# Optimization experiments

Measured on AMD Instinct MI355X. Metric: run time of the kernel, lower is better.

The kernel has to match this reference:

```python
import jax, jax.numpy as jnp
import numpy as np

INPUT_DIM, HIDDEN, CB_DIM, CB_SIZE = 768, 512, 256, 512
COMMIT_W = 1.0


def setup_inputs() -> dict:
    key = jax.random.key(0)
    ks = jax.random.split(key, 10)
    def lin(k, fan_in, fan_out):
        lim = 1.0 / np.sqrt(fan_in)
        return jax.random.uniform(k, (fan_in, fan_out), jnp.float32, -lim, lim)
    return {
        "x": jax.random.normal(ks[0], (32, 2048, INPUT_DIM), jnp.float32),
        "W1": lin(ks[1], INPUT_DIM, HIDDEN),
        "b1": jnp.zeros((HIDDEN,), jnp.float32),
        "W2": lin(ks[2], HIDDEN, CB_DIM),
        "b2": jnp.zeros((CB_DIM,), jnp.float32),
        "codebook": jax.random.normal(ks[3], (CB_SIZE, CB_DIM), jnp.float32),
        "W3": lin(ks[4], CB_DIM, HIDDEN),
        "b3": jnp.zeros((HIDDEN,), jnp.float32),
        "W4": lin(ks[5], HIDDEN, INPUT_DIM),
        "b4": jnp.zeros((INPUT_DIM,), jnp.float32),
    }


def reference(x, W1, b1, W2, b2, codebook, W3, b3, W4, b4):
    # encoder MLP: [b, n, 768] -> [b, n, 256]
    h = jax.nn.relu(jnp.einsum('bnd,dh->bnh', x, W1) + b1)
    z = jnp.einsum('bnh,hc->bnc', h, W2) + b2

    # VQ: squared-L2 distance to codebook, argmin, gather
    # d(z, c) = ||z||^2 - 2 z.c + ||c||^2  (||z||^2 constant over argmin, omitted)
    dots = jnp.einsum('bnc,kc->bnk', z, codebook)          # [b, n, K]
    c_sq = jnp.sum(codebook * codebook, axis=-1)            # [K]
    indices = jnp.argmin(c_sq - 2.0 * dots, axis=-1)        # [b, n] int
    q = codebook[indices]                                   # [b, n, 256] gather

    # straight-through estimator + commitment loss
    quantized = z + jax.lax.stop_gradient(q - z)
    commit_loss = COMMIT_W * jnp.mean((z - jax.lax.stop_gradient(q)) ** 2)

    # decoder MLP: [b, n, 256] -> [b, n, 768]
    h2 = jax.nn.relu(jnp.einsum('bnc,ch->bnh', quantized, W3) + b3)
    recon = jnp.einsum('bnh,hd->bnd', h2, W4) + b4
    return recon, indices.astype(jnp.int32), commit_loss
```

## Files before the change

### kernel.cpp

```cpp
#include <hip/hip_runtime.h>

typedef unsigned short u16;
typedef unsigned int   u32;
typedef __attribute__((ext_vector_type(8))) short short8;
typedef __attribute__((ext_vector_type(4))) float f32x4;

#define NTOK 65536
#define IND  768
#define HID  512
#define CBD  256
#define CBS  512

#define OUT_IDX_OFF   ((size_t)NTOK * IND)
#define OUT_LOSS_OFF  (OUT_IDX_OFF + NTOK)

#define OFF_H      ((size_t)0)
#define OFF_Z      ((size_t)134217728)
#define OFF_W1H    ((size_t)201326592)
#define OFF_W1L    ((size_t)202113024)
#define OFF_W2H    ((size_t)202899456)
#define OFF_W2L    ((size_t)203161600)
#define OFF_CBH    ((size_t)203423744)
#define OFF_CBL    ((size_t)203685888)
#define OFF_CSQ    ((size_t)203948032)
#define OFF_PART   ((size_t)0)
#define OFF_TABLE  ((size_t)8388608)
#define OFF_ZSQ    ((size_t)9961472)
#define OFF_IDX    ((size_t)10223616)
#define OFF_FLAGS  ((size_t)10485760)
#define OFF_CNT    ((size_t)10747904)

__device__ __forceinline__ u16 f2bf(float f) {
    u32 u = __float_as_uint(f);
    return (u16)((u + 0x7fffu + ((u >> 16) & 1u)) >> 16);
}
__device__ __forceinline__ float bf2f(u16 h) {
    return __uint_as_float(((u32)h) << 16);
}

__global__ __launch_bounds__(256) void cbsplit(
    const float* __restrict__ cb, u16* __restrict__ hi, u16* __restrict__ lo,
    float* __restrict__ csq)
{
    int c = blockIdx.x, t = threadIdx.x;
    float v = cb[(size_t)c * CBD + t];
    u16 h = f2bf(v); u16 l = f2bf(v - bf2f(h));
    hi[(size_t)c * CBD + t] = h; lo[(size_t)c * CBD + t] = l;
    __shared__ float red[256];
    red[t] = v * v; __syncthreads();
    for (int s = 128; s; s >>= 1) { if (t < s) red[t] += red[t + s]; __syncthreads(); }
    if (!t) csq[c] = red[0];
}

__global__ __launch_bounds__(256) void wsplit(
    const float* __restrict__ W, u16* __restrict__ hi, u16* __restrict__ lo,
    int K, int N)
{
    int n = blockIdx.x;
    for (int k = threadIdx.x; k < K; k += 256) {
        float v = W[(size_t)k * N + n];
        u16 h = f2bf(v); u16 l = f2bf(v - bf2f(h));
        hi[(size_t)n * K + k] = h; lo[(size_t)n * K + k] = l;
    }
}

template<int AMODE, int EPI>
__global__ __launch_bounds__(256, 2) void gemm3(
    const float* __restrict__ Af, const u32* __restrict__ Apk,
    const u16* __restrict__ Bhi, const u16* __restrict__ Blo,
    const float* __restrict__ bias,
    u32* __restrict__ Opk, float* __restrict__ Opart,
    int M, int N, int K)
{
    __shared__ u16 lds[4 * 128 * 40];
    u16* sAh = lds;
    u16* sAl = lds + 5120;
    u16* sBh = lds + 10240;
    u16* sBl = lds + 15360;
    const int tid  = threadIdx.x;
    const int m0 = blockIdx.y * 128, n0 = blockIdx.x * 128;
    const int w = tid >> 6, lane = tid & 63, quad = lane >> 4, l15 = lane & 15;
    const int wm = (w & 1) * 64, wn = (w >> 1) * 64;

    f32x4 acc[4][4] = {};

    for (int k0 = 0; k0 < K; k0 += 32) {
        __syncthreads();
        if (AMODE == 0) {
            #pragma unroll
            for (int s = 0; s < 4; ++s) {
                int slot = tid + s * 256;
                int m = slot >> 3, kg = (slot & 7) << 2;
                float4 v = *(const float4*)(Af + (size_t)(m0 + m) * K + k0 + kg);
                u16 h0 = f2bf(v.x), h1 = f2bf(v.y), h2 = f2bf(v.z), h3 = f2bf(v.w);
                ushort4 hv = {h0, h1, h2, h3};
                ushort4 lv = {f2bf(v.x - bf2f(h0)), f2bf(v.y - bf2f(h1)),
                              f2bf(v.z - bf2f(h2)), f2bf(v.w - bf2f(h3))};
                *(ushort4*)&sAh[m * 40 + kg] = hv;
                *(ushort4*)&sAl[m * 40 + kg] = lv;
            }
        } else {
            #pragma unroll
            for (int s = 0; s < 4; ++s) {
                int slot = tid + s * 256;
                int m = slot >> 3, ke = (slot & 7) << 2;
                uint4 u = *(const uint4*)(Apk + (size_t)(m0 + m) * K + k0 + ke);
                ushort4 hv = {(u16)(u.x & 0xffff), (u16)(u.y & 0xffff),
                              (u16)(u.z & 0xffff), (u16)(u.w & 0xffff)};
                ushort4 lv = {(u16)(u.x >> 16), (u16)(u.y >> 16),
                              (u16)(u.z >> 16), (u16)(u.w >> 16)};
                *(ushort4*)&sAh[m * 40 + ke] = hv;
                *(ushort4*)&sAl[m * 40 + ke] = lv;
            }
        }
        #pragma unroll
        for (int s = 0; s < 4; ++s) {
            int slot = tid + s * 256;
            int n = (slot & 511) >> 2, ku = slot & 3;
            const u16* src = (slot < 512) ? Bhi : Blo;
            u16* dst = (slot < 512) ? sBh : sBl;
            uint4 u = *(const uint4*)(src + (size_t)(n0 + n) * K + k0 + ku * 8);
            *(uint4*)&dst[n * 40 + ku * 8] = u;
        }
        __syncthreads();

        short8 ah[4], al[4], bh[4], bl[4];
        const int ko = quad * 8;
        #pragma unroll
        for (int i = 0; i < 4; ++i) {
            int ar = wm + i * 16 + l15;
            int br = wn + i * 16 + l15;
            ah[i] = *(const short8*)&sAh[ar * 40 + ko];
            al[i] = *(const short8*)&sAl[ar * 40 + ko];
            bh[i] = *(const short8*)&sBh[br * 40 + ko];
            bl[i] = *(const short8*)&sBl[br * 40 + ko];
        }
        #pragma unroll
        for (int i = 0; i < 4; ++i)
            #pragma unroll
            for (int j = 0; j < 4; ++j) {
                acc[i][j] = __builtin_amdgcn_mfma_f32_16x16x32_bf16(ah[i], bh[j], acc[i][j], 0, 0, 0);
                acc[i][j] = __builtin_amdgcn_mfma_f32_16x16x32_bf16(ah[i], bl[j], acc[i][j], 0, 0, 0);
                acc[i][j] = __builtin_amdgcn_mfma_f32_16x16x32_bf16(al[i], bh[j], acc[i][j], 0, 0, 0);
            }
    }

    if (EPI <= 1) {
        float bn[4];
        #pragma unroll
        for (int j = 0; j < 4; ++j) bn[j] = bias[n0 + wn + j * 16 + l15];
        #pragma unroll
        for (int i = 0; i < 4; ++i)
            #pragma unroll
            for (int r = 0; r < 4; ++r) {
                int row = m0 + wm + i * 16 + quad * 4 + r;
                #pragma unroll
                for (int j = 0; j < 4; ++j) {
                    float v = acc[i][j][r] + bn[j];
                    if (EPI == 0) v = fmaxf(v, 0.f);
                    u16 h = f2bf(v); u16 l = f2bf(v - bf2f(h));
                    Opk[(size_t)row * N + n0 + wn + j * 16 + l15] = (u32)h | ((u32)l << 16);
                }
            }
    } else {
        float cs[4]; int cidx[4];
        #pragma unroll
        for (int j = 0; j < 4; ++j) {
            cidx[j] = n0 + wn + j * 16 + l15;
            cs[j] = bias[cidx[j]];
        }
        const int nparts = gridDim.x * 2;
        const int pslot  = blockIdx.x * 2 + (w >> 1);
        #pragma unroll
        for (int i = 0; i < 4; ++i)
            #pragma unroll
            for (int r = 0; r < 4; ++r) {
                int row = m0 + wm + i * 16 + quad * 4 + r;
                float d1 = 3.4e38f, d2 = 3.4e38f; int i1 = 0x7fffffff;
                #pragma unroll
                for (int j = 0; j < 4; ++j) {
                    float v = fmaf(-2.0f, acc[i][j][r], cs[j]);
                    if (v < d1) { d2 = d1; d1 = v; i1 = cidx[j]; }
                    else d2 = fminf(d2, v);
                }
                #pragma unroll
                for (int mm = 1; mm < 16; mm <<= 1) {
                    float od1 = __shfl_xor(d1, mm, 64);
                    float od2 = __shfl_xor(d2, mm, 64);
                    int   oi1 = __shfl_xor(i1, mm, 64);
                    if (od1 < d1 || (od1 == d1 && oi1 < i1)) { d2 = fminf(d1, od2); d1 = od1; i1 = oi1; }
                    else d2 = fminf(d2, od1);
                }
                if (l15 == 0) {
                    float4 o = {d1, d2, __int_as_float(i1), 0.f};
                    *(float4*)&Opart[((size_t)row * nparts + pslot) * 4] = o;
                }
            }
    }
}

__global__ __launch_bounds__(256) void zsq_pk(
    const u32* __restrict__ Zpk, float* __restrict__ zsq)
{
    int tok = blockIdx.x * 4 + (threadIdx.x >> 6);
    int lane = threadIdx.x & 63;
    uint4 u = *(const uint4*)(Zpk + (size_t)tok * CBD + lane * 4);
    float z0 = bf2f((u16)(u.x & 0xffff)) + bf2f((u16)(u.x >> 16));
    float z1 = bf2f((u16)(u.y & 0xffff)) + bf2f((u16)(u.y >> 16));
    float z2 = bf2f((u16)(u.z & 0xffff)) + bf2f((u16)(u.z >> 16));
    float z3 = bf2f((u16)(u.w & 0xffff)) + bf2f((u16)(u.w >> 16));
    float s = z0 * z0 + z1 * z1 + z2 * z2 + z3 * z3;
    #pragma unroll
    for (int off = 32; off; off >>= 1) s += __shfl_down(s, off, 64);
    if (!lane) zsq[tok] = s;
}

__global__ __launch_bounds__(256) void vq_reduce(
    const float* __restrict__ part, const float* __restrict__ zsq,
    float* __restrict__ out_idx, int* __restrict__ idx_i,
    int* __restrict__ cnt, float* __restrict__ accum, int* __restrict__ flags)
{
    int tok = blockIdx.x * 256 + threadIdx.x;
    float d1 = 3.4e38f, d2 = 3.4e38f; int i1 = 0x7fffffff;
    #pragma unroll
    for (int nb = 0; nb < 8; ++nb) {
        float4 p = *(const float4*)&part[((size_t)tok * 8 + nb) * 4];
        float pd1 = p.x, pd2 = p.y; int pi1 = __float_as_int(p.z);
        if (pd1 < d1 || (pd1 == d1 && pi1 < i1)) { d2 = fminf(d1, pd2); d1 = pd1; i1 = pi1; }
        else d2 = fminf(d2, pd1);
    }
    out_idx[tok] = (float)i1;
    idx_i[tok] = i1;
    if (d2 - d1 < 0.05f) {
        int p = atomicAdd(cnt, 1);
        if (p >= 0 && p < NTOK) flags[p] = tok;
    }
    float c = zsq[tok] + d1;
    __shared__ float red[256];
    red[threadIdx.x] = c; __syncthreads();
    for (int s = 128; s; s >>= 1) { if (threadIdx.x < s) red[threadIdx.x] += red[threadIdx.x + s]; __syncthreads(); }
    if (!threadIdx.x) atomicAdd(accum, red[0]);
}

__global__ __launch_bounds__(256) void fixup(
    const int* __restrict__ cnt, const int* __restrict__ flags,
    const float* __restrict__ x, const float* __restrict__ W1, const float* __restrict__ b1,
    const float* __restrict__ W2, const float* __restrict__ b2,
    const float* __restrict__ cb, const float* __restrict__ csq,
    int* __restrict__ idx_i, float* __restrict__ out_idx)
{
    __shared__ float xs[IND], hs[HID], zs[CBD], ds[CBS];
    int n = cnt[0]; if (n > NTOK) n = NTOK; if (n < 0) n = 0;
    int t = threadIdx.x;
    for (int it = blockIdx.x; it < n; it += gridDim.x) {
        int tok = flags[it];
        if (t < 192) *(float4*)&xs[t * 4] = *(const float4*)(x + (size_t)tok * IND + t * 4);
        __syncthreads();
        #pragma unroll
        for (int s2 = 0; s2 < 2; ++s2) {
            int j = t + s2 * 256; float a = b1[j];
            for (int k = 0; k < IND; ++k) a = fmaf(xs[k], W1[(size_t)k * HID + j], a);
            hs[j] = fmaxf(a, 0.f);
        }
        __syncthreads();
        {
            float a = b2[t];
            for (int k = 0; k < HID; ++k) a = fmaf(hs[k], W2[(size_t)k * CBD + t], a);
            zs[t] = a;
        }
        __syncthreads();
        {
            int wv = t >> 6, l = t & 63;
            float4 zv = *(const float4*)&zs[l * 4];
            for (int cc = 0; cc < 128; ++cc) {
                int c = wv * 128 + cc;
                float4 cv = *(const float4*)(cb + (size_t)c * CBD + l * 4);
                float p = zv.x * cv.x + zv.y * cv.y + zv.z * cv.z + zv.w * cv.w;
                #pragma unroll
                for (int mm = 32; mm; mm >>= 1) p += __shfl_xor(p, mm, 64);
                if (!l) ds[c] = csq[c] - 2.f * p;
            }
        }
        __syncthreads();
        if (t < 64) {
            float bd = ds[t]; int bi = t;
            for (int c = t + 64; c < CBS; c += 64) {
                float d = ds[c];
                if (d < bd || (d == bd && c < bi)) { bd = d; bi = c; }
            }
            #pragma unroll
            for (int mm = 1; mm < 64; mm <<= 1) {
                float od = __shfl_xor(bd, mm, 64); int oi = __shfl_xor(bi, mm, 64);
                if (od < bd || (od == bd && oi < bi)) { bd = od; bi = oi; }
            }
            if (!t) { idx_i[tok] = bi; out_idx[tok] = (float)bi; }
        }
        __syncthreads();
    }
}

__global__ __launch_bounds__(256) void table_pre(
    const float* __restrict__ cb, const float* __restrict__ W3,
    const float* __restrict__ b3, const float* __restrict__ W4,
    const float* __restrict__ b4, float* __restrict__ table)
{
    __shared__ float crow[CBD];
    __shared__ float h2[HID];
    const int c = blockIdx.x;
    const int t = threadIdx.x;
    crow[t] = cb[(size_t)c * CBD + t];
    __syncthreads();
    #pragma unroll
    for (int s = 0; s < 2; ++s) {
        int j = t + s * 256;
        float acc = b3[j];
        for (int k = 0; k < CBD; ++k) acc = fmaf(crow[k], W3[(size_t)k * HID + j], acc);
        h2[j] = fmaxf(acc, 0.f);
    }
    __syncthreads();
    #pragma unroll
    for (int s = 0; s < 3; ++s) {
        int j = t + s * 256;
        float acc = b4[j];
        for (int k = 0; k < HID; ++k) acc = fmaf(h2[k], W4[(size_t)k * IND + j], acc);
        table[(size_t)c * IND + j] = acc;
    }
}

__global__ __launch_bounds__(256) void gather_kernel(
    const int* __restrict__ idx, const float* __restrict__ table,
    float* __restrict__ out)
{
    unsigned i = blockIdx.x * 256u + threadIdx.x;
    unsigned tok = i / 192u;
    unsigned c = i - tok * 192u;
    int id = idx[tok];
    ((float4*)out)[i] = ((const float4*)table)[(size_t)id * 192 + c];
}

__global__ void finalize_kernel(const float* __restrict__ accum,
                                float* __restrict__ out_loss)
{
    out_loss[0] = accum[0] * (1.0f / 16777216.0f);
}

extern "C" void kernel_launch(void* const* d_in, const int* in_sizes, int n_in,
                              void* d_out, int out_size, void* d_ws, size_t ws_size,
                              hipStream_t stream) {
    const float* x  = (const float*)d_in[0];
    const float* W1 = (const float*)d_in[1];
    const float* b1 = (const float*)d_in[2];
    const float* W2 = (const float*)d_in[3];
    const float* b2 = (const float*)d_in[4];
    const float* cb = (const float*)d_in[5];
    const float* W3 = (const float*)d_in[6];
    const float* b3 = (const float*)d_in[7];
    const float* W4 = (const float*)d_in[8];
    const float* b4 = (const float*)d_in[9];

    char* ws = (char*)d_ws;
    u32*  Hpk   = (u32*)(ws + OFF_H);
    u32*  Zpk   = (u32*)(ws + OFF_Z);
    u16*  W1h   = (u16*)(ws + OFF_W1H);
    u16*  W1l   = (u16*)(ws + OFF_W1L);
    u16*  W2h   = (u16*)(ws + OFF_W2H);
    u16*  W2l   = (u16*)(ws + OFF_W2L);
    u16*  CBh   = (u16*)(ws + OFF_CBH);
    u16*  CBl   = (u16*)(ws + OFF_CBL);
    float* csq  = (float*)(ws + OFF_CSQ);
    float* part = (float*)(ws + OFF_PART);
    float* table = (float*)(ws + OFF_TABLE);
    float* zsq  = (float*)(ws + OFF_ZSQ);
    int*   idx_i = (int*)(ws + OFF_IDX);
    int*   flags = (int*)(ws + OFF_FLAGS);
    int*   cnt   = (int*)(ws + OFF_CNT);
    float* accum = (float*)(ws + OFF_CNT + 4);

    float* out      = (float*)d_out;
    float* out_idx  = out + OUT_IDX_OFF;
    float* out_loss = out + OUT_LOSS_OFF;

    cbsplit<<<CBS, 256, 0, stream>>>(cb, CBh, CBl, csq);
    wsplit<<<HID, 256, 0, stream>>>(W1, W1h, W1l, IND, HID);
    wsplit<<<CBD, 256, 0, stream>>>(W2, W2h, W2l, HID, CBD);

    gemm3<0, 0><<<dim3(HID / 128, NTOK / 128), 256, 0, stream>>>(
        x, (const u32*)nullptr, W1h, W1l, b1, Hpk, (float*)nullptr, NTOK, HID, IND);
    gemm3<1, 1><<<dim3(CBD / 128, NTOK / 128), 256, 0, stream>>>(
        (const float*)nullptr, Hpk, W2h, W2l, b2, Zpk, (float*)nullptr, NTOK, CBD, HID);

    hipMemsetAsync(cnt, 0, 8, stream);

    zsq_pk<<<NTOK / 4, 256, 0, stream>>>(Zpk, zsq);

    gemm3<1, 2><<<dim3(CBS / 128, NTOK / 128), 256, 0, stream>>>(
        (const float*)nullptr, Zpk, CBh, CBl, csq, (u32*)nullptr, part, NTOK, CBS, CBD);

    table_pre<<<CBS, 256, 0, stream>>>(cb, W3, b3, W4, b4, table);

    vq_reduce<<<NTOK / 256, 256, 0, stream>>>(part, zsq, out_idx, idx_i, cnt, accum, flags);

    fixup<<<192, 256, 0, stream>>>(cnt, flags, x, W1, b1, W2, b2, cb, csq, idx_i, out_idx);

    gather_kernel<<<(NTOK * (IND / 4)) / 256, 256, 0, stream>>>(idx_i, table, out);

    finalize_kernel<<<1, 1, 0, stream>>>(accum, out_loss);
}
```

Baseline: 1.019 ms.

## Batch eight flagged tokens per block in FP32 VQ fixup kernel

The fixup kernel recomputes the encoder and codebook argmin in exact FP32 for tokens whose top-two distances are close. It now handles eight tokens per block iteration, so each W1, W2 and codebook element loaded from global memory is reused across eight tokens instead of one. The argmin now runs as a per-wave running minimum instead of going through a shared distance array. The launch grid grows from 192 to 1024 blocks. Shared memory per block and register pressure rise, and when few tokens are flagged the padded batches do redundant work.

After: 984.9 us. 3.4% less time.

```diff
diff --git a/kernel.cpp b/kernel.cpp
--- a/kernel.cpp
+++ b/kernel.cpp
@@ -249,51 +249,115 @@
     const float* __restrict__ cb, const float* __restrict__ csq,
     int* __restrict__ idx_i, float* __restrict__ out_idx)
 {
-    __shared__ float xs[IND], hs[HID], zs[CBD], ds[CBS];
+    __shared__ float xs[8][IND];
+    __shared__ float hs[8][HID];
+    __shared__ float zs[8][CBD];
+    __shared__ float bd_s[4][8];
+    __shared__ int   bi_s[4][8];
+    __shared__ int   tok_s[8];
+
     int n = cnt[0]; if (n > NTOK) n = NTOK; if (n < 0) n = 0;
-    int t = threadIdx.x;
-    for (int it = blockIdx.x; it < n; it += gridDim.x) {
-        int tok = flags[it];
-        if (t < 192) *(float4*)&xs[t * 4] = *(const float4*)(x + (size_t)tok * IND + t * 4);
-        __syncthreads();
-        #pragma unroll
-        for (int s2 = 0; s2 < 2; ++s2) {
-            int j = t + s2 * 256; float a = b1[j];
-            for (int k = 0; k < IND; ++k) a = fmaf(xs[k], W1[(size_t)k * HID + j], a);
-            hs[j] = fmaxf(a, 0.f);
-        }
-        __syncthreads();
+    const int t = threadIdx.x;
+    const int nb = (n + 7) >> 3;
+
+    for (int ib = blockIdx.x; ib < nb; ib += gridDim.x) {
+        const int base = ib * 8;
+        if (t < 8) {
+            int fi = base + t; if (fi > n - 1) fi = n - 1;
+            tok_s[t] = flags[fi];
+        }
+        __syncthreads();
+
+        #pragma unroll
+        for (int s = 0; s < 6; ++s) {
+            int slot = t + s * 256;
+            int tt = slot / 192, c4 = slot - tt * 192;
+            *(float4*)&xs[tt][c4 * 4] =
+                *(const float4*)(x + (size_t)tok_s[tt] * IND + c4 * 4);
+        }
+        __syncthreads();
+
         {
-            float a = b2[t];
-            for (int k = 0; k < HID; ++k) a = fmaf(hs[k], W2[(size_t)k * CBD + t], a);
-            zs[t] = a;
-        }
-        __syncthreads();
+            float a0[8], a1[8];
+            float bb0 = b1[t], bb1 = b1[t + 256];
+            #pragma unroll
+            for (int tt = 0; tt < 8; ++tt) { a0[tt] = bb0; a1[tt] = bb1; }
+            #pragma unroll 4
+            for (int k = 0; k < IND; ++k) {
+                float w0 = W1[(size_t)k * HID + t];
+                float w1 = W1[(size_t)k * HID + t + 256];
+                #pragma unroll
+                for (int tt = 0; tt < 8; ++tt) {
+                    float xv = xs[tt][k];
+                    a0[tt] = fmaf(xv, w0, a0[tt]);
+                    a1[tt] = fmaf(xv, w1, a1[tt]);
+                }
+            }
+            #pragma unroll
+            for (int tt = 0; tt < 8; ++tt) {
+                hs[tt][t]       = fmaxf(a0[tt], 0.f);
+                hs[tt][t + 256] = fmaxf(a1[tt], 0.f);
+            }
+        }
+        __syncthreads();
+
         {
-            int wv = t >> 6, l = t & 63;
-            float4 zv = *(const float4*)&zs[l * 4];
+            float az[8];
+            float bz = b2[t];
+            #pragma unroll
+            for (int tt = 0; tt < 8; ++tt) az[tt] = bz;
+            #pragma unroll 4
+            for (int k = 0; k < HID; ++k) {
+                float w = W2[(size_t)k * CBD + t];
+                #pragma unroll
+                for (int tt = 0; tt < 8; ++tt)
+                    az[tt] = fmaf(hs[tt][k], w, az[tt]);
+            }
+            #pragma unroll
+            for (int tt = 0; tt < 8; ++tt) zs[tt][t] = az[tt];
+        }
+        __syncthreads();
+
+        {
+            const int wv = t >> 6, l = t & 63;
+            float4 zv[8];
+            #pragma unroll
+            for (int tt = 0; tt < 8; ++tt) zv[tt] = *(const float4*)&zs[tt][l * 4];
+            float bd[8]; int bi[8];
+            #pragma unroll
+            for (int tt = 0; tt < 8; ++tt) { bd[tt] = 3.4e38f; bi[tt] = 0x7fffffff; }
             for (int cc = 0; cc < 128; ++cc) {
                 int c = wv * 128 + cc;
                 float4 cv = *(const float4*)(cb + (size_t)c * CBD + l * 4);
-                float p = zv.x * cv.x + zv.y * cv.y + zv.z * cv.z + zv.w * cv.w;
-                #pragma unroll
-                for (int mm = 32; mm; mm >>= 1) p += __shfl_xor(p, mm, 64);
-                if (!l) ds[c] = csq[c] - 2.f * p;
-            }
-        }
-        __syncthreads();
-        if (t < 64) {
-            float bd = ds[t]; int bi = t;
-            for (int c = t + 64; c < CBS; c += 64) {
-                float d = ds[c];
-                if (d < bd || (d == bd && c < bi)) { bd = d; bi = c; }
-            }
-            #pragma unroll
-            for (int mm = 1; mm < 64; mm <<= 1) {
-                float od = __shfl_xor(bd, mm, 64); int oi = __shfl_xor(bi, mm, 64);
-                if (od < bd || (od == bd && oi < bi)) { bd = od; bi = oi; }
-            }
-            if (!t) { idx_i[tok] = bi; out_idx[tok] = (float)bi; }
+                float cs = csq[c];
+                #pragma unroll
+                for (int tt = 0; tt < 8; ++tt) {
+                    float p = zv[tt].x * cv.x + zv[tt].y * cv.y + zv[tt].z * cv.z + zv[tt].w * cv.w;
+                    #pragma unroll
+                    for (int mm = 32; mm; mm >>= 1) p += __shfl_xor(p, mm, 64);
+                    float d = cs - 2.f * p;
+                    if (d < bd[tt]) { bd[tt] = d; bi[tt] = c; }
+                }
+            }
+            if (l == 0) {
+                #pragma unroll
+                for (int tt = 0; tt < 8; ++tt) { bd_s[wv][tt] = bd[tt]; bi_s[wv][tt] = bi[tt]; }
+            }
+        }
+        __syncthreads();
+
+        if (t < 8) {
+            const int tt = t;
+            float d = bd_s[0][tt]; int i = bi_s[0][tt];
+            #pragma unroll
+            for (int wv = 1; wv < 4; ++wv) {
+                float od = bd_s[wv][tt]; int oi = bi_s[wv][tt];
+                if (od < d || (od == d && oi < i)) { d = od; i = oi; }
+            }
+            if (base + tt < n) {
+                int tok = tok_s[tt];
+                idx_i[tok] = i; out_idx[tok] = (float)i;
+            }
         }
         __syncthreads();
     }
@@ -400,7 +464,7 @@
 
     vq_reduce<<<NTOK / 256, 256, 0, stream>>>(part, zsq, out_idx, idx_i, cnt, accum, flags);
 
-    fixup<<<192, 256, 0, stream>>>(cnt, flags, x, W1, b1, W2, b2, cb, csq, idx_i, out_idx);
+    fixup<<<1024, 256, 0, stream>>>(cnt, flags, x, W1, b1, W2, b2, cb, csq, idx_i, out_idx);
 
     gather_kernel<<<(NTOK * (IND / 4)) / 256, 256, 0, stream>>>(idx_i, table, out);
 
```
